# Kernel optimization log

Hardware: AMD Instinct MI355X
Metric: run time of the kernel (lower is better)

Reference implementation:

```python
import jax, jax.numpy as jnp
import numpy as np

N = 50000
E = 800000
IN_CH = 256
HID = 32
HEADS = 4
OUT_CH = 40
NEG_SLOPE = 0.2
BN_EPS = 1e-5


def _gat_conv(x, W, att_src, att_dst, bias, src, dst, num_nodes, concat):
    # x: [N, F_in]; W: [F_in, H*C]; att_src/att_dst: [H, C]
    H, C = att_src.shape
    h = (x @ W).reshape(num_nodes, H, C)            # [N, H, C]
    a_src = (h * att_src[None]).sum(-1)             # [N, H]
    a_dst = (h * att_dst[None]).sum(-1)             # [N, H]
    e = jax.nn.leaky_relu(a_src[src] + a_dst[dst], NEG_SLOPE)  # [Etot, H]
    # segment softmax over incoming edges of each destination node
    m = jax.ops.segment_max(e, dst, num_segments=num_nodes)    # [N, H]
    ex = jnp.exp(e - m[dst])
    s = jax.ops.segment_sum(ex, dst, num_segments=num_nodes)   # [N, H]
    alpha = ex / (s[dst] + 1e-16)                   # [Etot, H]
    out = jax.ops.segment_sum(h[src] * alpha[:, :, None], dst,
                              num_segments=num_nodes)          # [N, H, C]
    out = out.reshape(num_nodes, H * C) if concat else out.mean(axis=1)
    return out + bias


def setup_inputs() -> dict:
    key = jax.random.key(0)
    ks = jax.random.split(key, 12)
    x = jax.random.normal(ks[0], (N, IN_CH), dtype=jnp.float32)
    edge_index = jax.random.randint(ks[1], (2, E), 0, N, dtype=jnp.int64)
    # layer 1: in -> heads*hid, concat
    W1 = jax.random.normal(ks[2], (IN_CH, HEADS * HID), dtype=jnp.float32) * (1.0 / np.sqrt(IN_CH))
    att_src1 = jax.random.normal(ks[3], (HEADS, HID), dtype=jnp.float32) * 0.1
    att_dst1 = jax.random.normal(ks[4], (HEADS, HID), dtype=jnp.float32) * 0.1
    b1 = jnp.zeros((HEADS * HID,), dtype=jnp.float32)
    # batch norm over hidden*heads features
    gamma = jnp.ones((HEADS * HID,), dtype=jnp.float32)
    beta = jnp.zeros((HEADS * HID,), dtype=jnp.float32)
    # layer 2: heads*hid -> out, heads=1, mean (concat=False)
    W2 = jax.random.normal(ks[5], (HEADS * HID, OUT_CH), dtype=jnp.float32) * (1.0 / np.sqrt(HEADS * HID))
    att_src2 = jax.random.normal(ks[6], (1, OUT_CH), dtype=jnp.float32) * 0.1
    att_dst2 = jax.random.normal(ks[7], (1, OUT_CH), dtype=jnp.float32) * 0.1
    b2 = jnp.zeros((OUT_CH,), dtype=jnp.float32)
    return {"x": x, "edge_index": edge_index, "W1": W1, "att_src1": att_src1,
            "att_dst1": att_dst1, "b1": b1, "gamma": gamma, "beta": beta,
            "W2": W2, "att_src2": att_src2, "att_dst2": att_dst2, "b2": b2}


def reference(x, edge_index, W1, att_src1, att_dst1, b1, gamma, beta,
              W2, att_src2, att_dst2, b2):
    num_nodes = x.shape[0]
    loops = jnp.arange(num_nodes, dtype=edge_index.dtype)
    src = jnp.concatenate([edge_index[0], loops])   # add self-loops (PyG default)
    dst = jnp.concatenate([edge_index[1], loops])
    h = _gat_conv(x, W1, att_src1, att_dst1, b1, src, dst, num_nodes, concat=True)
    # BatchNorm over nodes (training-mode batch statistics)
    mu = h.mean(axis=0)
    var = h.var(axis=0)
    h = (h - mu) * jax.lax.rsqrt(var + BN_EPS) * gamma + beta
    h = jax.nn.elu(h)
    out = _gat_conv(h, W2, att_src2, att_dst2, b2, src, dst, num_nodes, concat=False)
    return out
```

## Files before the change

kernel.cpp:

```cpp
#include <hip/hip_runtime.h>

#define NN 50000
#define EE 800000
#define FIN 256
#define F1 128
#define F2 40
#define CAP 48
#define G1B ((NN + 63) / 64)
#define FILLB ((EE + 255) / 256)
#define G1PB 3126
#define G2B ((NN + 15) / 16)
#define LSTR 56

typedef unsigned int u32;
typedef unsigned short u16;
typedef _Float16 h8 __attribute__((ext_vector_type(8)));
typedef float f4 __attribute__((ext_vector_type(4)));

static __device__ __forceinline__ u32 f2bf(float f) {
  u32 u = __float_as_uint(f);
  return (u + 0x7FFFu + ((u >> 16) & 1u)) >> 16;
}
#define BF_LO(u) __uint_as_float((u) << 16)
#define BF_HI(u) __uint_as_float((u) & 0xFFFF0000u)

__global__ __launch_bounds__(256) void g1f_kernel(const float* __restrict__ x,
                                                  const float* __restrict__ W1,
                                                  const float* __restrict__ att_src,
                                                  const float* __restrict__ att_dst,
                                                  u32* __restrict__ h1bf,
                                                  float* __restrict__ a_src,
                                                  float* __restrict__ a_dst,
                                                  const int* __restrict__ ei,
                                                  int* __restrict__ cnt,
                                                  int* __restrict__ csr) {
  __shared__ __align__(16) _Float16 Alds[64 * LSTR];
  __shared__ __align__(16) _Float16 Blds[128 * LSTR];
  const int t = threadIdx.x;

  if (blockIdx.x >= G1B) {
    int e = (blockIdx.x - G1B) * 256 + t;
    if (e < EE) {
      int src = ei[e];
      int dst = ei[EE + e];
      int p = atomicAdd(cnt + dst, 1);
      if (p < CAP) csr[dst * CAP + p] = src;
    }
    return;
  }

  const int m0 = blockIdx.x * 64;
  const int l  = t & 63;
  const int w  = t >> 6;
  const int q  = l & 15;
  const int hq = l >> 4;

  const int arow  = t >> 2;
  const int akoff = (t & 3) * 8;
  const int bn    = t & 127;
  const int bkh   = (t >> 7) * 16;

  f4 acc[8] = {};

  float ax[8];
  float bx[16];
  {
    int gr = m0 + arow;
    if (gr < NN) {
      float4 u0 = *(const float4*)(x + (size_t)gr * FIN + akoff);
      float4 u1 = *(const float4*)(x + (size_t)gr * FIN + akoff + 4);
      ax[0] = u0.x; ax[1] = u0.y; ax[2] = u0.z; ax[3] = u0.w;
      ax[4] = u1.x; ax[5] = u1.y; ax[6] = u1.z; ax[7] = u1.w;
    } else {
#pragma unroll
      for (int i = 0; i < 8; ++i) ax[i] = 0.f;
    }
#pragma unroll
    for (int i = 0; i < 16; ++i) bx[i] = W1[(size_t)(bkh + i) * F1 + bn];
  }

  for (int s = 0; s < 8; ++s) {
    __syncthreads();
    {
      h8 av;
#pragma unroll
      for (int i = 0; i < 8; ++i) av[i] = (_Float16)ax[i];
      *(h8*)(Alds + arow * LSTR + akoff) = av;
      h8 bv0, bv1;
#pragma unroll
      for (int i = 0; i < 8; ++i) { bv0[i] = (_Float16)bx[i]; bv1[i] = (_Float16)bx[8 + i]; }
      *(h8*)(Blds + bn * LSTR + bkh) = bv0;
      *(h8*)(Blds + bn * LSTR + bkh + 8) = bv1;
    }
    __syncthreads();
    if (s < 7) {
      int k0 = (s + 1) * 32;
      int gr = m0 + arow;
      if (gr < NN) {
        float4 u0 = *(const float4*)(x + (size_t)gr * FIN + k0 + akoff);
        float4 u1 = *(const float4*)(x + (size_t)gr * FIN + k0 + akoff + 4);
        ax[0] = u0.x; ax[1] = u0.y; ax[2] = u0.z; ax[3] = u0.w;
        ax[4] = u1.x; ax[5] = u1.y; ax[6] = u1.z; ax[7] = u1.w;
      } else {
#pragma unroll
        for (int i = 0; i < 8; ++i) ax[i] = 0.f;
      }
#pragma unroll
      for (int i = 0; i < 16; ++i) bx[i] = W1[(size_t)(k0 + bkh + i) * F1 + bn];
    }
    h8 af = *(const h8*)(Alds + (w * 16 + q) * LSTR + hq * 8);
#pragma unroll
    for (int nf = 0; nf < 8; ++nf) {
      h8 bf = *(const h8*)(Blds + (nf * 16 + q) * LSTR + hq * 8);
      acc[nf] = __builtin_amdgcn_mfma_f32_16x16x32_f16(af, bf, acc[nf], 0, 0, 0);
    }
  }

  u16* h1u = (u16*)h1bf;
#pragma unroll
  for (int nf = 0; nf < 8; ++nf) {
    int ph = nf >> 1;
#pragma unroll
    for (int r = 0; r < 4; ++r) {
      int grow = m0 + w * 16 + hq * 4 + r;
      if (grow < NN)
        h1u[((size_t)ph * NN + grow) * 32 + (nf & 1) * 16 + q] = (u16)f2bf(acc[nf][r]);
    }
  }
  float as8[8], ad8[8];
#pragma unroll
  for (int nf = 0; nf < 8; ++nf) {
    as8[nf] = att_src[nf * 16 + q];
    ad8[nf] = att_dst[nf * 16 + q];
  }
#pragma unroll
  for (int r = 0; r < 4; ++r) {
    float p0 = acc[0][r] * as8[0] + acc[1][r] * as8[1];
    float p1 = acc[2][r] * as8[2] + acc[3][r] * as8[3];
    float p2 = acc[4][r] * as8[4] + acc[5][r] * as8[5];
    float p3 = acc[6][r] * as8[6] + acc[7][r] * as8[7];
    float d0 = acc[0][r] * ad8[0] + acc[1][r] * ad8[1];
    float d1 = acc[2][r] * ad8[2] + acc[3][r] * ad8[3];
    float d2 = acc[4][r] * ad8[4] + acc[5][r] * ad8[5];
    float d3 = acc[6][r] * ad8[6] + acc[7][r] * ad8[7];
#pragma unroll
    for (int off = 1; off < 16; off <<= 1) {
      p0 += __shfl_xor(p0, off); p1 += __shfl_xor(p1, off);
      p2 += __shfl_xor(p2, off); p3 += __shfl_xor(p3, off);
      d0 += __shfl_xor(d0, off); d1 += __shfl_xor(d1, off);
      d2 += __shfl_xor(d2, off); d3 += __shfl_xor(d3, off);
    }
    int grow = m0 + w * 16 + hq * 4 + r;
    if (grow < NN && q < 8) {
      float vs = (q & 2) ? ((q & 1) ? p3 : p2) : ((q & 1) ? p1 : p0);
      float vd = (q & 2) ? ((q & 1) ? d3 : d2) : ((q & 1) ? d1 : d0);
      if (q < 4) a_src[grow * 4 + q] = vs;
      else       a_dst[grow * 4 + (q - 4)] = vd;
    }
  }
}

__global__ __launch_bounds__(256) void gather1_kernel(const int* __restrict__ cnt,
                                                      const int* __restrict__ csr,
                                                      const float* __restrict__ a_src,
                                                      const float* __restrict__ a_dst,
                                                      const u32* __restrict__ h1bf,
                                                      const float* __restrict__ b1,
                                                      float* __restrict__ h1b,
                                                      float* __restrict__ bnsum,
                                                      float* __restrict__ bnsq) {
  __shared__ float bns[32], bnq[32];
  int t = threadIdx.x;
  if (t < 32) { bns[t] = 0.f; bnq[t] = 0.f; }
  __syncthreads();
  int d = blockIdx.x;
  int xcd = d & 7;
  int p = xcd >> 1;
  int nb = ((d >> 3) << 1) + (xcd & 1);
  int n = nb * 16 + (t >> 4);
  int sub = t & 15;
  int g = sub >> 2;
  int l = sub & 3;
  int f0 = p * 32 + l * 8;
  float acc[8] = {0.f, 0.f, 0.f, 0.f, 0.f, 0.f, 0.f, 0.f};
  float ssum = 0.f;
  if (n < NN) {
    float adst = a_dst[n * 4 + p];
    const u32* hb = h1bf + (size_t)p * NN * 16 + l * 4;
    if (g == 0) {
      float e0 = a_src[n * 4 + p] + adst;
      e0 = e0 > 0.f ? e0 : 0.2f * e0;
      float x0 = __expf(e0);
      uint4 qv = *(const uint4*)(hb + (size_t)n * 16);
      acc[0] = fmaf(x0, BF_LO(qv.x), acc[0]); acc[1] = fmaf(x0, BF_HI(qv.x), acc[1]);
      acc[2] = fmaf(x0, BF_LO(qv.y), acc[2]); acc[3] = fmaf(x0, BF_HI(qv.y), acc[3]);
      acc[4] = fmaf(x0, BF_LO(qv.z), acc[4]); acc[5] = fmaf(x0, BF_HI(qv.z), acc[5]);
      acc[6] = fmaf(x0, BF_LO(qv.w), acc[6]); acc[7] = fmaf(x0, BF_HI(qv.w), acc[7]);
      ssum += x0;
    }
    const int* row = csr + n * CAP;
    int m = cnt[n]; if (m > CAP) m = CAP;
    int i = g;
    for (; i + 4 < m; i += 8) {
      int s0 = row[i];
      int s1 = row[i + 4];
      float e0 = a_src[s0 * 4 + p] + adst;
      float e1 = a_src[s1 * 4 + p] + adst;
      uint4 q0 = *(const uint4*)(hb + (size_t)s0 * 16);
      uint4 q1 = *(const uint4*)(hb + (size_t)s1 * 16);
      e0 = e0 > 0.f ? e0 : 0.2f * e0;  float x0 = __expf(e0);
      e1 = e1 > 0.f ? e1 : 0.2f * e1;  float x1 = __expf(e1);
      acc[0] = fmaf(x0, BF_LO(q0.x), acc[0]); acc[1] = fmaf(x0, BF_HI(q0.x), acc[1]);
      acc[2] = fmaf(x0, BF_LO(q0.y), acc[2]); acc[3] = fmaf(x0, BF_HI(q0.y), acc[3]);
      acc[4] = fmaf(x0, BF_LO(q0.z), acc[4]); acc[5] = fmaf(x0, BF_HI(q0.z), acc[5]);
      acc[6] = fmaf(x0, BF_LO(q0.w), acc[6]); acc[7] = fmaf(x0, BF_HI(q0.w), acc[7]);
      acc[0] = fmaf(x1, BF_LO(q1.x), acc[0]); acc[1] = fmaf(x1, BF_HI(q1.x), acc[1]);
      acc[2] = fmaf(x1, BF_LO(q1.y), acc[2]); acc[3] = fmaf(x1, BF_HI(q1.y), acc[3]);
      acc[4] = fmaf(x1, BF_LO(q1.z), acc[4]); acc[5] = fmaf(x1, BF_HI(q1.z), acc[5]);
      acc[6] = fmaf(x1, BF_LO(q1.w), acc[6]); acc[7] = fmaf(x1, BF_HI(q1.w), acc[7]);
      ssum += x0 + x1;
    }
    for (; i < m; i += 4) {
      int s0 = row[i];
      float e0 = a_src[s0 * 4 + p] + adst;
      e0 = e0 > 0.f ? e0 : 0.2f * e0;
      float x0 = __expf(e0);
      uint4 qv = *(const uint4*)(hb + (size_t)s0 * 16);
      acc[0] = fmaf(x0, BF_LO(qv.x), acc[0]); acc[1] = fmaf(x0, BF_HI(qv.x), acc[1]);
      acc[2] = fmaf(x0, BF_LO(qv.y), acc[2]); acc[3] = fmaf(x0, BF_HI(qv.y), acc[3]);
      acc[4] = fmaf(x0, BF_LO(qv.z), acc[4]); acc[5] = fmaf(x0, BF_HI(qv.z), acc[5]);
      acc[6] = fmaf(x0, BF_LO(qv.w), acc[6]); acc[7] = fmaf(x0, BF_HI(qv.w), acc[7]);
      ssum += x0;
    }
  }
#pragma unroll
  for (int j = 0; j < 8; ++j) {
    acc[j] += __shfl_xor(acc[j], 4);
    acc[j] += __shfl_xor(acc[j], 8);
  }
  ssum += __shfl_xor(ssum, 4);
  ssum += __shfl_xor(ssum, 8);
  if (n < NN && g == 0) {
    float inv = 1.f / (ssum + 1e-16f);
    float4 b0 = *(const float4*)(b1 + f0);
    float4 b4 = *(const float4*)(b1 + f0 + 4);
    float o[8];
    o[0] = acc[0] * inv + b0.x; o[1] = acc[1] * inv + b0.y;
    o[2] = acc[2] * inv + b0.z; o[3] = acc[3] * inv + b0.w;
    o[4] = acc[4] * inv + b4.x; o[5] = acc[5] * inv + b4.y;
    o[6] = acc[6] * inv + b4.z; o[7] = acc[7] * inv + b4.w;
    float4 w0 = {o[0], o[1], o[2], o[3]};
    float4 w1 = {o[4], o[5], o[6], o[7]};
    *(float4*)(h1b + (size_t)n * F1 + f0) = w0;
    *(float4*)(h1b + (size_t)n * F1 + f0 + 4) = w1;
    int lb = l * 8;
#pragma unroll
    for (int j = 0; j < 8; ++j) {
      atomicAdd(&bns[lb + j], o[j]);
      atomicAdd(&bnq[lb + j], o[j] * o[j]);
    }
  }
  __syncthreads();
  if (t < 32) {
    atomicAdd(bnsum + p * 32 + t, bns[t]);
    atomicAdd(bnsq + p * 32 + t, bnq[t]);
  }
}

__global__ __launch_bounds__(256) void gemm2_kernel(const float* __restrict__ hpre,
                                                    const float* __restrict__ W2,
                                                    const float* __restrict__ bnsum,
                                                    const float* __restrict__ bnsq,
                                                    const float* __restrict__ gamma,
                                                    const float* __restrict__ beta,
                                                    u16* __restrict__ h2a,
                                                    u16* __restrict__ h2b,
                                                    const float* __restrict__ att_src2,
                                                    const float* __restrict__ att_dst2,
                                                    float* __restrict__ a_src2,
                                                    float* __restrict__ a_dst2) {
  __shared__ float Wlds[128 * 40];
  __shared__ float Alds[16 * 128];
  __shared__ float sc[128], sh[128];
  int t = threadIdx.x;
  for (int i = t; i < 128 * 40; i += 256) Wlds[i] = W2[i];
  if (t < 128) {
    const float invN = 1.f / (float)NN;
    float mu = bnsum[t] * invN;
    float var = bnsq[t] * invN - mu * mu;
    float s = gamma[t] * rsqrtf(var + 1e-5f);
    sc[t] = s;
    sh[t] = beta[t] - mu * s;
  }
  int tr = t >> 3;
  int tc = t & 7;
  float as5[5], ad5[5];
#pragma unroll
  for (int j = 0; j < 5; ++j) { as5[j] = att_src2[tc * 5 + j]; ad5[j] = att_dst2[tc * 5 + j]; }
  int n0 = blockIdx.x * 128;
  int lrow = t >> 1;
  int lkk = (t & 1) * 8;
  float acc[4][5];
#pragma unroll
  for (int i = 0; i < 4; ++i)
#pragma unroll
    for (int j = 0; j < 5; ++j) acc[i][j] = 0.f;

  for (int k0 = 0; k0 < F1; k0 += 16) {
    float av[8];
    int gn = n0 + lrow;
    if (gn < NN) {
      float4 v0 = *(const float4*)(hpre + (size_t)gn * F1 + k0 + lkk);
      float4 v1 = *(const float4*)(hpre + (size_t)gn * F1 + k0 + lkk + 4);
      av[0] = v0.x; av[1] = v0.y; av[2] = v0.z; av[3] = v0.w;
      av[4] = v1.x; av[5] = v1.y; av[6] = v1.z; av[7] = v1.w;
    } else {
#pragma unroll
      for (int j = 0; j < 8; ++j) av[j] = 0.f;
    }
    __syncthreads();
#pragma unroll
    for (int j = 0; j < 8; ++j) {
      int kg = k0 + lkk + j;
      float a = av[j] * sc[kg] + sh[kg];
      a = a > 0.f ? a : (__expf(a) - 1.f);
      Alds[(lkk + j) * 128 + lrow] = a;
    }
    __syncthreads();
#pragma unroll
    for (int k = 0; k < 16; ++k) {
      float4 a4 = *(const float4*)(Alds + k * 128 + tr * 4);
      float aa[4] = {a4.x, a4.y, a4.z, a4.w};
      float w[5];
#pragma unroll
      for (int j = 0; j < 5; ++j) w[j] = Wlds[(k0 + k) * 40 + tc * 5 + j];
#pragma unroll
      for (int i = 0; i < 4; ++i)
#pragma unroll
        for (int j = 0; j < 5; ++j) acc[i][j] = fmaf(aa[i], w[j], acc[i][j]);
    }
  }
#pragma unroll
  for (int i = 0; i < 4; ++i) {
    int gn = n0 + tr * 4 + i;
    if (gn < NN) {
#pragma unroll
      for (int j = 0; j < 5; ++j) {
        int f = tc * 5 + j;
        u16 v = (u16)f2bf(acc[i][j]);
        if (f < 32) h2a[(size_t)gn * 32 + f] = v;
        else        h2b[(size_t)gn * 8 + (f - 32)] = v;
      }
    }
  }
#pragma unroll
  for (int i = 0; i < 4; ++i) {
    float ps = 0.f, pd = 0.f;
#pragma unroll
    for (int j = 0; j < 5; ++j) { ps += acc[i][j] * as5[j]; pd += acc[i][j] * ad5[j]; }
#pragma unroll
    for (int off = 1; off < 8; off <<= 1) {
      ps += __shfl_xor(ps, off);
      pd += __shfl_xor(pd, off);
    }
    if (tc == 0) {
      int gn = n0 + tr * 4 + i;
      if (gn < NN) { a_src2[gn] = ps; a_dst2[gn] = pd; }
    }
  }
}

__global__ __launch_bounds__(256) void gather2_kernel(const int* __restrict__ cnt,
                                                      const int* __restrict__ csr,
                                                      const float* __restrict__ a_src,
                                                      const float* __restrict__ a_dst,
                                                      const u32* __restrict__ h2a,
                                                      const u32* __restrict__ h2b,
                                                      const float* __restrict__ b2,
                                                      float* __restrict__ out) {
  int t = threadIdx.x;
  int n = blockIdx.x * 16 + (t >> 4);
  if (n >= NN) return;
  int l = t & 7;
  int g = (t >> 3) & 1;
  bool act = (l < 5);
  bool isA = (l < 4);
  float adst = a_dst[n];
  float acc[8] = {0.f, 0.f, 0.f, 0.f, 0.f, 0.f, 0.f, 0.f};
  float ssum = 0.f;
  const uint4 zz = {0u, 0u, 0u, 0u};
  if (g == 0) {
    float e0 = a_src[n] + adst;
    e0 = e0 > 0.f ? e0 : 0.2f * e0;
    float x0 = __expf(e0);
    uint4 q = act ? (isA ? *(const uint4*)(h2a + (size_t)n * 16 + l * 4)
                         : *(const uint4*)(h2b + (size_t)n * 4)) : zz;
    acc[0] = fmaf(x0, BF_LO(q.x), acc[0]); acc[1] = fmaf(x0, BF_HI(q.x), acc[1]);
    acc[2] = fmaf(x0, BF_LO(q.y), acc[2]); acc[3] = fmaf(x0, BF_HI(q.y), acc[3]);
    acc[4] = fmaf(x0, BF_LO(q.z), acc[4]); acc[5] = fmaf(x0, BF_HI(q.z), acc[5]);
    acc[6] = fmaf(x0, BF_LO(q.w), acc[6]); acc[7] = fmaf(x0, BF_HI(q.w), acc[7]);
    ssum += x0;
  }
  const int* row = csr + n * CAP;
  int m = cnt[n]; if (m > CAP) m = CAP;
  for (int c = 4 * g; c < m; c += 8) {
    if (c + 4 <= m) {
      int4 s4 = *(const int4*)(row + c);
      float e0 = a_src[s4.x] + adst;
      float e1 = a_src[s4.y] + adst;
      float e2 = a_src[s4.z] + adst;
      float e3 = a_src[s4.w] + adst;
      uint4 q0 = act ? (isA ? *(const uint4*)(h2a + (size_t)s4.x * 16 + l * 4)
                            : *(const uint4*)(h2b + (size_t)s4.x * 4)) : zz;
      uint4 q1 = act ? (isA ? *(const uint4*)(h2a + (size_t)s4.y * 16 + l * 4)
                            : *(const uint4*)(h2b + (size_t)s4.y * 4)) : zz;
      uint4 q2 = act ? (isA ? *(const uint4*)(h2a + (size_t)s4.z * 16 + l * 4)
                            : *(const uint4*)(h2b + (size_t)s4.z * 4)) : zz;
      uint4 q3 = act ? (isA ? *(const uint4*)(h2a + (size_t)s4.w * 16 + l * 4)
                            : *(const uint4*)(h2b + (size_t)s4.w * 4)) : zz;
      e0 = e0 > 0.f ? e0 : 0.2f * e0;  float x0 = __expf(e0);
      e1 = e1 > 0.f ? e1 : 0.2f * e1;  float x1 = __expf(e1);
      e2 = e2 > 0.f ? e2 : 0.2f * e2;  float x2 = __expf(e2);
      e3 = e3 > 0.f ? e3 : 0.2f * e3;  float x3 = __expf(e3);
      acc[0] = fmaf(x0, BF_LO(q0.x), acc[0]); acc[1] = fmaf(x0, BF_HI(q0.x), acc[1]);
      acc[2] = fmaf(x0, BF_LO(q0.y), acc[2]); acc[3] = fmaf(x0, BF_HI(q0.y), acc[3]);
      acc[4] = fmaf(x0, BF_LO(q0.z), acc[4]); acc[5] = fmaf(x0, BF_HI(q0.z), acc[5]);
      acc[6] = fmaf(x0, BF_LO(q0.w), acc[6]); acc[7] = fmaf(x0, BF_HI(q0.w), acc[7]);
      acc[0] = fmaf(x1, BF_LO(q1.x), acc[0]); acc[1] = fmaf(x1, BF_HI(q1.x), acc[1]);
      acc[2] = fmaf(x1, BF_LO(q1.y), acc[2]); acc[3] = fmaf(x1, BF_HI(q1.y), acc[3]);
      acc[4] = fmaf(x1, BF_LO(q1.z), acc[4]); acc[5] = fmaf(x1, BF_HI(q1.z), acc[5]);
      acc[6] = fmaf(x1, BF_LO(q1.w), acc[6]); acc[7] = fmaf(x1, BF_HI(q1.w), acc[7]);
      acc[0] = fmaf(x2, BF_LO(q2.x), acc[0]); acc[1] = fmaf(x2, BF_HI(q2.x), acc[1]);
      acc[2] = fmaf(x2, BF_LO(q2.y), acc[2]); acc[3] = fmaf(x2, BF_HI(q2.y), acc[3]);
      acc[4] = fmaf(x2, BF_LO(q2.z), acc[4]); acc[5] = fmaf(x2, BF_HI(q2.z), acc[5]);
      acc[6] = fmaf(x2, BF_LO(q2.w), acc[6]); acc[7] = fmaf(x2, BF_HI(q2.w), acc[7]);
      acc[0] = fmaf(x3, BF_LO(q3.x), acc[0]); acc[1] = fmaf(x3, BF_HI(q3.x), acc[1]);
      acc[2] = fmaf(x3, BF_LO(q3.y), acc[2]); acc[3] = fmaf(x3, BF_HI(q3.y), acc[3]);
      acc[4] = fmaf(x3, BF_LO(q3.z), acc[4]); acc[5] = fmaf(x3, BF_HI(q3.z), acc[5]);
      acc[6] = fmaf(x3, BF_LO(q3.w), acc[6]); acc[7] = fmaf(x3, BF_HI(q3.w), acc[7]);
      ssum += x0 + x1 + x2 + x3;
    } else {
      for (int i = c; i < m; ++i) {
        int s0 = row[i];
        float e0 = a_src[s0] + adst;
        e0 = e0 > 0.f ? e0 : 0.2f * e0;
        float x0 = __expf(e0);
        uint4 q = act ? (isA ? *(const uint4*)(h2a + (size_t)s0 * 16 + l * 4)
                             : *(const uint4*)(h2b + (size_t)s0 * 4)) : zz;
        acc[0] = fmaf(x0, BF_LO(q.x), acc[0]); acc[1] = fmaf(x0, BF_HI(q.x), acc[1]);
        acc[2] = fmaf(x0, BF_LO(q.y), acc[2]); acc[3] = fmaf(x0, BF_HI(q.y), acc[3]);
        acc[4] = fmaf(x0, BF_LO(q.z), acc[4]); acc[5] = fmaf(x0, BF_HI(q.z), acc[5]);
        acc[6] = fmaf(x0, BF_LO(q.w), acc[6]); acc[7] = fmaf(x0, BF_HI(q.w), acc[7]);
        ssum += x0;
      }
    }
  }
#pragma unroll
  for (int j = 0; j < 8; ++j) acc[j] += __shfl_xor(acc[j], 8);
  ssum += __shfl_xor(ssum, 8);
  float inv = 1.f / (ssum + 1e-16f);
  if (g == 0 && act) {
    float* op = out + (size_t)n * F2 + l * 8;
#pragma unroll
    for (int j = 0; j < 8; ++j) op[j] = acc[j] * inv + b2[l * 8 + j];
  }
}

extern "C" void kernel_launch(void* const* d_in, const int* in_sizes, int n_in,
                              void* d_out, int out_size, void* d_ws, size_t ws_size,
                              hipStream_t stream) {
  const float* x        = (const float*)d_in[0];
  const int*   ei       = (const int*)d_in[1];
  const float* W1       = (const float*)d_in[2];
  const float* att_src1 = (const float*)d_in[3];
  const float* att_dst1 = (const float*)d_in[4];
  const float* b1       = (const float*)d_in[5];
  const float* gamma    = (const float*)d_in[6];
  const float* beta     = (const float*)d_in[7];
  const float* W2       = (const float*)d_in[8];
  const float* att_src2 = (const float*)d_in[9];
  const float* att_dst2 = (const float*)d_in[10];
  const float* b2       = (const float*)d_in[11];
  float* out = (float*)d_out;

  int* cnt      = (int*)d_ws;
  float* bnsum  = (float*)(cnt + 50048);
  float* bnsq   = bnsum + 128;
  int* csr      = (int*)(bnsq + 128);
  u32* h1bf     = (u32*)(csr + NN * CAP);
  float* h1b    = (float*)(h1bf + 3200000);
  u32* h2a      = (u32*)(h1b + 6400000);
  u32* h2b      = h2a + 800000;
  float* a_src1 = (float*)(h2b + 200000);
  float* a_dst1 = a_src1 + 200000;
  float* a_src2 = a_dst1 + 200000;
  float* a_dst2 = a_src2 + 50000;

  hipMemsetAsync(cnt, 0, (50048 + 256) * sizeof(int), stream);

  g1f_kernel<<<G1B + FILLB, 256, 0, stream>>>(x, W1, att_src1, att_dst1,
                                              h1bf, a_src1, a_dst1,
                                              ei, cnt, csr);
  gather1_kernel<<<(G1PB / 2) * 8, 256, 0, stream>>>(cnt, csr, a_src1, a_dst1,
                                                     h1bf, b1, h1b, bnsum, bnsq);
  gemm2_kernel<<<(NN + 127) / 128, 256, 0, stream>>>(h1b, W2, bnsum, bnsq,
                                                     gamma, beta,
                                                     (u16*)h2a, (u16*)h2b,
                                                     att_src2, att_dst2,
                                                     a_src2, a_dst2);
  gather2_kernel<<<G2B, 256, 0, stream>>>(cnt, csr, a_src2, a_dst2,
                                          h2a, h2b, b2, out);
}
```

Before: 313.1 us.

## Store layer-1 features row-major and gather all heads per node in one block

```diff
diff --git a/kernel.cpp b/kernel.cpp
--- a/kernel.cpp
+++ b/kernel.cpp
@@ -8,7 +8,6 @@
 #define CAP 48
 #define G1B ((NN + 63) / 64)
 #define FILLB ((EE + 255) / 256)
-#define G1PB 3126
 #define G2B ((NN + 15) / 16)
 #define LSTR 56
 
@@ -23,6 +22,12 @@
 }
 #define BF_LO(u) __uint_as_float((u) << 16)
 #define BF_HI(u) __uint_as_float((u) & 0xFFFF0000u)
+
+static __device__ __forceinline__ float sel4(float4 v, int h) {
+  float a = (h & 1) ? v.y : v.x;
+  float b = (h & 1) ? v.w : v.z;
+  return (h & 2) ? b : a;
+}
 
 __global__ __launch_bounds__(256) void g1f_kernel(const float* __restrict__ x,
                                                   const float* __restrict__ W1,
@@ -119,12 +124,11 @@
   u16* h1u = (u16*)h1bf;
 #pragma unroll
   for (int nf = 0; nf < 8; ++nf) {
-    int ph = nf >> 1;
 #pragma unroll
     for (int r = 0; r < 4; ++r) {
       int grow = m0 + w * 16 + hq * 4 + r;
       if (grow < NN)
-        h1u[((size_t)ph * NN + grow) * 32 + (nf & 1) * 16 + q] = (u16)f2bf(acc[nf][r]);
+        h1u[(size_t)grow * 128 + nf * 16 + q] = (u16)f2bf(acc[nf][r]);
     }
   }
   float as8[8], ad8[8];
@@ -169,101 +173,86 @@
                                                       float* __restrict__ h1b,
                                                       float* __restrict__ bnsum,
                                                       float* __restrict__ bnsq) {
-  __shared__ float bns[32], bnq[32];
+  __shared__ float bns[128], bnq[128];
   int t = threadIdx.x;
-  if (t < 32) { bns[t] = 0.f; bnq[t] = 0.f; }
+  if (t < 128) { bns[t] = 0.f; bnq[t] = 0.f; }
   __syncthreads();
-  int d = blockIdx.x;
-  int xcd = d & 7;
-  int p = xcd >> 1;
-  int nb = ((d >> 3) << 1) + (xcd & 1);
-  int n = nb * 16 + (t >> 4);
-  int sub = t & 15;
-  int g = sub >> 2;
-  int l = sub & 3;
-  int f0 = p * 32 + l * 8;
+  int n = blockIdx.x * 16 + (t >> 4);
+  int l = t & 15;
+  int h = l >> 2;
+  float adst = sel4(*(const float4*)(a_dst + n * 4), h);
   float acc[8] = {0.f, 0.f, 0.f, 0.f, 0.f, 0.f, 0.f, 0.f};
   float ssum = 0.f;
-  if (n < NN) {
-    float adst = a_dst[n * 4 + p];
-    const u32* hb = h1bf + (size_t)p * NN * 16 + l * 4;
-    if (g == 0) {
-      float e0 = a_src[n * 4 + p] + adst;
-      e0 = e0 > 0.f ? e0 : 0.2f * e0;
-      float x0 = __expf(e0);
-      uint4 qv = *(const uint4*)(hb + (size_t)n * 16);
-      acc[0] = fmaf(x0, BF_LO(qv.x), acc[0]); acc[1] = fmaf(x0, BF_HI(qv.x), acc[1]);
-      acc[2] = fmaf(x0, BF_LO(qv.y), acc[2]); acc[3] = fmaf(x0, BF_HI(qv.y), acc[3]);
-      acc[4] = fmaf(x0, BF_LO(qv.z), acc[4]); acc[5] = fmaf(x0, BF_HI(qv.z), acc[5]);
-      acc[6] = fmaf(x0, BF_LO(qv.w), acc[6]); acc[7] = fmaf(x0, BF_HI(qv.w), acc[7]);
-      ssum += x0;
-    }
-    const int* row = csr + n * CAP;
-    int m = cnt[n]; if (m > CAP) m = CAP;
-    int i = g;
-    for (; i + 4 < m; i += 8) {
-      int s0 = row[i];
-      int s1 = row[i + 4];
-      float e0 = a_src[s0 * 4 + p] + adst;
-      float e1 = a_src[s1 * 4 + p] + adst;
-      uint4 q0 = *(const uint4*)(hb + (size_t)s0 * 16);
-      uint4 q1 = *(const uint4*)(hb + (size_t)s1 * 16);
-      e0 = e0 > 0.f ? e0 : 0.2f * e0;  float x0 = __expf(e0);
-      e1 = e1 > 0.f ? e1 : 0.2f * e1;  float x1 = __expf(e1);
-      acc[0] = fmaf(x0, BF_LO(q0.x), acc[0]); acc[1] = fmaf(x0, BF_HI(q0.x), acc[1]);
-      acc[2] = fmaf(x0, BF_LO(q0.y), acc[2]); acc[3] = fmaf(x0, BF_HI(q0.y), acc[3]);
-      acc[4] = fmaf(x0, BF_LO(q0.z), acc[4]); acc[5] = fmaf(x0, BF_HI(q0.z), acc[5]);
-      acc[6] = fmaf(x0, BF_LO(q0.w), acc[6]); acc[7] = fmaf(x0, BF_HI(q0.w), acc[7]);
-      acc[0] = fmaf(x1, BF_LO(q1.x), acc[0]); acc[1] = fmaf(x1, BF_HI(q1.x), acc[1]);
-      acc[2] = fmaf(x1, BF_LO(q1.y), acc[2]); acc[3] = fmaf(x1, BF_HI(q1.y), acc[3]);
-      acc[4] = fmaf(x1, BF_LO(q1.z), acc[4]); acc[5] = fmaf(x1, BF_HI(q1.z), acc[5]);
-      acc[6] = fmaf(x1, BF_LO(q1.w), acc[6]); acc[7] = fmaf(x1, BF_HI(q1.w), acc[7]);
-      ssum += x0 + x1;
-    }
-    for (; i < m; i += 4) {
-      int s0 = row[i];
-      float e0 = a_src[s0 * 4 + p] + adst;
-      e0 = e0 > 0.f ? e0 : 0.2f * e0;
-      float x0 = __expf(e0);
-      uint4 qv = *(const uint4*)(hb + (size_t)s0 * 16);
-      acc[0] = fmaf(x0, BF_LO(qv.x), acc[0]); acc[1] = fmaf(x0, BF_HI(qv.x), acc[1]);
-      acc[2] = fmaf(x0, BF_LO(qv.y), acc[2]); acc[3] = fmaf(x0, BF_HI(qv.y), acc[3]);
-      acc[4] = fmaf(x0, BF_LO(qv.z), acc[4]); acc[5] = fmaf(x0, BF_HI(qv.z), acc[5]);
-      acc[6] = fmaf(x0, BF_LO(qv.w), acc[6]); acc[7] = fmaf(x0, BF_HI(qv.w), acc[7]);
-      ssum += x0;
-    }
-  }
+  const u32* hb = h1bf + l * 4;
+  {
+    float e0 = sel4(*(const float4*)(a_src + n * 4), h) + adst;
+    e0 = e0 > 0.f ? e0 : 0.2f * e0;
+    float x0 = __expf(e0);
+    uint4 qv = *(const uint4*)(hb + (size_t)n * 64);
+    acc[0] = fmaf(x0, BF_LO(qv.x), acc[0]); acc[1] = fmaf(x0, BF_HI(qv.x), acc[1]);
+    acc[2] = fmaf(x0, BF_LO(qv.y), acc[2]); acc[3] = fmaf(x0, BF_HI(qv.y), acc[3]);
+    acc[4] = fmaf(x0, BF_LO(qv.z), acc[4]); acc[5] = fmaf(x0, BF_HI(qv.z), acc[5]);
+    acc[6] = fmaf(x0, BF_LO(qv.w), acc[6]); acc[7] = fmaf(x0, BF_HI(qv.w), acc[7]);
+    ssum += x0;
+  }
+  const int* row = csr + n * CAP;
+  int m = cnt[n]; if (m > CAP) m = CAP;
+  int i = 0;
+  for (; i + 1 < m; i += 2) {
+    int s0 = row[i];
+    int s1 = row[i + 1];
+    float4 v0 = *(const float4*)(a_src + s0 * 4);
+    float4 v1 = *(const float4*)(a_src + s1 * 4);
+    uint4 q0 = *(const uint4*)(hb + (size_t)s0 * 64);
+    uint4 q1 = *(const uint4*)(hb + (size_t)s1 * 64);
+    float e0 = sel4(v0, h) + adst;
+    float e1 = sel4(v1, h) + adst;
+    e0 = e0 > 0.f ? e0 : 0.2f * e0;  float x0 = __expf(e0);
+    e1 = e1 > 0.f ? e1 : 0.2f * e1;  float x1 = __expf(e1);
+    acc[0] = fmaf(x0, BF_LO(q0.x), acc[0]); acc[1] = fmaf(x0, BF_HI(q0.x), acc[1]);
+    acc[2] = fmaf(x0, BF_LO(q0.y), acc[2]); acc[3] = fmaf(x0, BF_HI(q0.y), acc[3]);
+    acc[4] = fmaf(x0, BF_LO(q0.z), acc[4]); acc[5] = fmaf(x0, BF_HI(q0.z), acc[5]);
+    acc[6] = fmaf(x0, BF_LO(q0.w), acc[6]); acc[7] = fmaf(x0, BF_HI(q0.w), acc[7]);
+    acc[0] = fmaf(x1, BF_LO(q1.x), acc[0]); acc[1] = fmaf(x1, BF_HI(q1.x), acc[1]);
+    acc[2] = fmaf(x1, BF_LO(q1.y), acc[2]); acc[3] = fmaf(x1, BF_HI(q1.y), acc[3]);
+    acc[4] = fmaf(x1, BF_LO(q1.z), acc[4]); acc[5] = fmaf(x1, BF_HI(q1.z), acc[5]);
+    acc[6] = fmaf(x1, BF_LO(q1.w), acc[6]); acc[7] = fmaf(x1, BF_HI(q1.w), acc[7]);
+    ssum += x0 + x1;
+  }
+  if (i < m) {
+    int s0 = row[i];
+    float e0 = sel4(*(const float4*)(a_src + s0 * 4), h) + adst;
+    e0 = e0 > 0.f ? e0 : 0.2f * e0;
+    float x0 = __expf(e0);
+    uint4 qv = *(const uint4*)(hb + (size_t)s0 * 64);
+    acc[0] = fmaf(x0, BF_LO(qv.x), acc[0]); acc[1] = fmaf(x0, BF_HI(qv.x), acc[1]);
+    acc[2] = fmaf(x0, BF_LO(qv.y), acc[2]); acc[3] = fmaf(x0, BF_HI(qv.y), acc[3]);
+    acc[4] = fmaf(x0, BF_LO(qv.z), acc[4]); acc[5] = fmaf(x0, BF_HI(qv.z), acc[5]);
+    acc[6] = fmaf(x0, BF_LO(qv.w), acc[6]); acc[7] = fmaf(x0, BF_HI(qv.w), acc[7]);
+    ssum += x0;
+  }
+  float inv = 1.f / (ssum + 1e-16f);
+  int f0 = l * 8;
+  float4 b0 = *(const float4*)(b1 + f0);
+  float4 b4 = *(const float4*)(b1 + f0 + 4);
+  float o[8];
+  o[0] = acc[0] * inv + b0.x; o[1] = acc[1] * inv + b0.y;
+  o[2] = acc[2] * inv + b0.z; o[3] = acc[3] * inv + b0.w;
+  o[4] = acc[4] * inv + b4.x; o[5] = acc[5] * inv + b4.y;
+  o[6] = acc[6] * inv + b4.z; o[7] = acc[7] * inv + b4.w;
+  float4 w0 = {o[0], o[1], o[2], o[3]};
+  float4 w1 = {o[4], o[5], o[6], o[7]};
+  *(float4*)(h1b + (size_t)n * F1 + f0) = w0;
+  *(float4*)(h1b + (size_t)n * F1 + f0 + 4) = w1;
 #pragma unroll
   for (int j = 0; j < 8; ++j) {
-    acc[j] += __shfl_xor(acc[j], 4);
-    acc[j] += __shfl_xor(acc[j], 8);
-  }
-  ssum += __shfl_xor(ssum, 4);
-  ssum += __shfl_xor(ssum, 8);
-  if (n < NN && g == 0) {
-    float inv = 1.f / (ssum + 1e-16f);
-    float4 b0 = *(const float4*)(b1 + f0);
-    float4 b4 = *(const float4*)(b1 + f0 + 4);
-    float o[8];
-    o[0] = acc[0] * inv + b0.x; o[1] = acc[1] * inv + b0.y;
-    o[2] = acc[2] * inv + b0.z; o[3] = acc[3] * inv + b0.w;
-    o[4] = acc[4] * inv + b4.x; o[5] = acc[5] * inv + b4.y;
-    o[6] = acc[6] * inv + b4.z; o[7] = acc[7] * inv + b4.w;
-    float4 w0 = {o[0], o[1], o[2], o[3]};
-    float4 w1 = {o[4], o[5], o[6], o[7]};
-    *(float4*)(h1b + (size_t)n * F1 + f0) = w0;
-    *(float4*)(h1b + (size_t)n * F1 + f0 + 4) = w1;
-    int lb = l * 8;
-#pragma unroll
-    for (int j = 0; j < 8; ++j) {
-      atomicAdd(&bns[lb + j], o[j]);
-      atomicAdd(&bnq[lb + j], o[j] * o[j]);
-    }
+    atomicAdd(&bns[f0 + j], o[j]);
+    atomicAdd(&bnq[f0 + j], o[j] * o[j]);
   }
   __syncthreads();
-  if (t < 32) {
-    atomicAdd(bnsum + p * 32 + t, bns[t]);
-    atomicAdd(bnsq + p * 32 + t, bnq[t]);
+  if (t < 128) {
+    atomicAdd(bnsum + t, bns[t]);
+    atomicAdd(bnsq + t, bnq[t]);
   }
 }
 
@@ -501,8 +490,8 @@
   g1f_kernel<<<G1B + FILLB, 256, 0, stream>>>(x, W1, att_src1, att_dst1,
                                               h1bf, a_src1, a_dst1,
                                               ei, cnt, csr);
-  gather1_kernel<<<(G1PB / 2) * 8, 256, 0, stream>>>(cnt, csr, a_src1, a_dst1,
-                                                     h1bf, b1, h1b, bnsum, bnsq);
+  gather1_kernel<<<G2B, 256, 0, stream>>>(cnt, csr, a_src1, a_dst1,
+                                          h1bf, b1, h1b, bnsum, bnsq);
   gemm2_kernel<<<(NN + 127) / 128, 256, 0, stream>>>(h1b, W2, bnsum, bnsq,
                                                      gamma, beta,
                                                      (u16*)h2a, (u16*)h2b,
```

Result: slower. 332.4 us (+6.2%).

## Compress CSR indices to 16-bit and split gather2 into head and tail block types

Applied to the files above, without the earlier changes.

```diff
diff --git a/kernel.cpp b/kernel.cpp
--- a/kernel.cpp
+++ b/kernel.cpp
@@ -9,7 +9,8 @@
 #define G1B ((NN + 63) / 64)
 #define FILLB ((EE + 255) / 256)
 #define G1PB 3126
-#define G2B ((NN + 15) / 16)
+#define G2P0 3125
+#define G2P1 ((NN + 63) / 64)
 #define LSTR 56
 
 typedef unsigned int u32;
@@ -33,7 +34,7 @@
                                                   float* __restrict__ a_dst,
                                                   const int* __restrict__ ei,
                                                   int* __restrict__ cnt,
-                                                  int* __restrict__ csr) {
+                                                  u16* __restrict__ csr) {
   __shared__ __align__(16) _Float16 Alds[64 * LSTR];
   __shared__ __align__(16) _Float16 Blds[128 * LSTR];
   const int t = threadIdx.x;
@@ -44,7 +45,7 @@
       int src = ei[e];
       int dst = ei[EE + e];
       int p = atomicAdd(cnt + dst, 1);
-      if (p < CAP) csr[dst * CAP + p] = src;
+      if (p < CAP) csr[dst * CAP + p] = (u16)src;
     }
     return;
   }
@@ -161,7 +162,7 @@
 }
 
 __global__ __launch_bounds__(256) void gather1_kernel(const int* __restrict__ cnt,
-                                                      const int* __restrict__ csr,
+                                                      const u16* __restrict__ csr,
                                                       const float* __restrict__ a_src,
                                                       const float* __restrict__ a_dst,
                                                       const u32* __restrict__ h1bf,
@@ -198,18 +199,18 @@
       acc[6] = fmaf(x0, BF_LO(qv.w), acc[6]); acc[7] = fmaf(x0, BF_HI(qv.w), acc[7]);
       ssum += x0;
     }
-    const int* row = csr + n * CAP;
+    const u16* row = csr + (size_t)n * CAP;
     int m = cnt[n]; if (m > CAP) m = CAP;
     int i = g;
     for (; i + 4 < m; i += 8) {
       int s0 = row[i];
       int s1 = row[i + 4];
-      float e0 = a_src[s0 * 4 + p] + adst;
-      float e1 = a_src[s1 * 4 + p] + adst;
+      float e0 = a_src[s0 * 4 + p];
+      float e1 = a_src[s1 * 4 + p];
       uint4 q0 = *(const uint4*)(hb + (size_t)s0 * 16);
       uint4 q1 = *(const uint4*)(hb + (size_t)s1 * 16);
-      e0 = e0 > 0.f ? e0 : 0.2f * e0;  float x0 = __expf(e0);
-      e1 = e1 > 0.f ? e1 : 0.2f * e1;  float x1 = __expf(e1);
+      e0 += adst; e0 = e0 > 0.f ? e0 : 0.2f * e0;  float x0 = __expf(e0);
+      e1 += adst; e1 = e1 > 0.f ? e1 : 0.2f * e1;  float x1 = __expf(e1);
       acc[0] = fmaf(x0, BF_LO(q0.x), acc[0]); acc[1] = fmaf(x0, BF_HI(q0.x), acc[1]);
       acc[2] = fmaf(x0, BF_LO(q0.y), acc[2]); acc[3] = fmaf(x0, BF_HI(q0.y), acc[3]);
       acc[4] = fmaf(x0, BF_LO(q0.z), acc[4]); acc[5] = fmaf(x0, BF_HI(q0.z), acc[5]);
@@ -371,7 +372,7 @@
 }
 
 __global__ __launch_bounds__(256) void gather2_kernel(const int* __restrict__ cnt,
-                                                      const int* __restrict__ csr,
+                                                      const u16* __restrict__ csr,
                                                       const float* __restrict__ a_src,
                                                       const float* __restrict__ a_dst,
                                                       const u32* __restrict__ h2a,
@@ -379,49 +380,39 @@
                                                       const float* __restrict__ b2,
                                                       float* __restrict__ out) {
   int t = threadIdx.x;
-  int n = blockIdx.x * 16 + (t >> 4);
-  if (n >= NN) return;
-  int l = t & 7;
-  int g = (t >> 3) & 1;
-  bool act = (l < 5);
-  bool isA = (l < 4);
-  float adst = a_dst[n];
-  float acc[8] = {0.f, 0.f, 0.f, 0.f, 0.f, 0.f, 0.f, 0.f};
-  float ssum = 0.f;
-  const uint4 zz = {0u, 0u, 0u, 0u};
-  if (g == 0) {
-    float e0 = a_src[n] + adst;
-    e0 = e0 > 0.f ? e0 : 0.2f * e0;
-    float x0 = __expf(e0);
-    uint4 q = act ? (isA ? *(const uint4*)(h2a + (size_t)n * 16 + l * 4)
-                         : *(const uint4*)(h2b + (size_t)n * 4)) : zz;
-    acc[0] = fmaf(x0, BF_LO(q.x), acc[0]); acc[1] = fmaf(x0, BF_HI(q.x), acc[1]);
-    acc[2] = fmaf(x0, BF_LO(q.y), acc[2]); acc[3] = fmaf(x0, BF_HI(q.y), acc[3]);
-    acc[4] = fmaf(x0, BF_LO(q.z), acc[4]); acc[5] = fmaf(x0, BF_HI(q.z), acc[5]);
-    acc[6] = fmaf(x0, BF_LO(q.w), acc[6]); acc[7] = fmaf(x0, BF_HI(q.w), acc[7]);
-    ssum += x0;
-  }
-  const int* row = csr + n * CAP;
-  int m = cnt[n]; if (m > CAP) m = CAP;
-  for (int c = 4 * g; c < m; c += 8) {
-    if (c + 4 <= m) {
-      int4 s4 = *(const int4*)(row + c);
-      float e0 = a_src[s4.x] + adst;
-      float e1 = a_src[s4.y] + adst;
-      float e2 = a_src[s4.z] + adst;
-      float e3 = a_src[s4.w] + adst;
-      uint4 q0 = act ? (isA ? *(const uint4*)(h2a + (size_t)s4.x * 16 + l * 4)
-                            : *(const uint4*)(h2b + (size_t)s4.x * 4)) : zz;
-      uint4 q1 = act ? (isA ? *(const uint4*)(h2a + (size_t)s4.y * 16 + l * 4)
-                            : *(const uint4*)(h2b + (size_t)s4.y * 4)) : zz;
-      uint4 q2 = act ? (isA ? *(const uint4*)(h2a + (size_t)s4.z * 16 + l * 4)
-                            : *(const uint4*)(h2b + (size_t)s4.z * 4)) : zz;
-      uint4 q3 = act ? (isA ? *(const uint4*)(h2a + (size_t)s4.w * 16 + l * 4)
-                            : *(const uint4*)(h2b + (size_t)s4.w * 4)) : zz;
-      e0 = e0 > 0.f ? e0 : 0.2f * e0;  float x0 = __expf(e0);
-      e1 = e1 > 0.f ? e1 : 0.2f * e1;  float x1 = __expf(e1);
-      e2 = e2 > 0.f ? e2 : 0.2f * e2;  float x2 = __expf(e2);
-      e3 = e3 > 0.f ? e3 : 0.2f * e3;  float x3 = __expf(e3);
+  int d = blockIdx.x;
+  if (d < G2P0) {
+    int n = d * 16 + (t >> 4);
+    int sub = t & 15;
+    int g = sub >> 2;
+    int l = sub & 3;
+    float adst = a_dst[n];
+    const u32* hb = h2a + l * 4;
+    float acc[8] = {0.f, 0.f, 0.f, 0.f, 0.f, 0.f, 0.f, 0.f};
+    float ssum = 0.f;
+    if (g == 0) {
+      float e0 = a_src[n] + adst;
+      e0 = e0 > 0.f ? e0 : 0.2f * e0;
+      float x0 = __expf(e0);
+      uint4 qv = *(const uint4*)(hb + (size_t)n * 16);
+      acc[0] = fmaf(x0, BF_LO(qv.x), acc[0]); acc[1] = fmaf(x0, BF_HI(qv.x), acc[1]);
+      acc[2] = fmaf(x0, BF_LO(qv.y), acc[2]); acc[3] = fmaf(x0, BF_HI(qv.y), acc[3]);
+      acc[4] = fmaf(x0, BF_LO(qv.z), acc[4]); acc[5] = fmaf(x0, BF_HI(qv.z), acc[5]);
+      acc[6] = fmaf(x0, BF_LO(qv.w), acc[6]); acc[7] = fmaf(x0, BF_HI(qv.w), acc[7]);
+      ssum += x0;
+    }
+    const u16* row = csr + (size_t)n * CAP;
+    int m = cnt[n]; if (m > CAP) m = CAP;
+    int i = g;
+    for (; i + 4 < m; i += 8) {
+      int s0 = row[i];
+      int s1 = row[i + 4];
+      float e0 = a_src[s0];
+      float e1 = a_src[s1];
+      uint4 q0 = *(const uint4*)(hb + (size_t)s0 * 16);
+      uint4 q1 = *(const uint4*)(hb + (size_t)s1 * 16);
+      e0 += adst; e0 = e0 > 0.f ? e0 : 0.2f * e0;  float x0 = __expf(e0);
+      e1 += adst; e1 = e1 > 0.f ? e1 : 0.2f * e1;  float x1 = __expf(e1);
       acc[0] = fmaf(x0, BF_LO(q0.x), acc[0]); acc[1] = fmaf(x0, BF_HI(q0.x), acc[1]);
       acc[2] = fmaf(x0, BF_LO(q0.y), acc[2]); acc[3] = fmaf(x0, BF_HI(q0.y), acc[3]);
       acc[4] = fmaf(x0, BF_LO(q0.z), acc[4]); acc[5] = fmaf(x0, BF_HI(q0.z), acc[5]);
@@ -430,39 +421,110 @@
       acc[2] = fmaf(x1, BF_LO(q1.y), acc[2]); acc[3] = fmaf(x1, BF_HI(q1.y), acc[3]);
       acc[4] = fmaf(x1, BF_LO(q1.z), acc[4]); acc[5] = fmaf(x1, BF_HI(q1.z), acc[5]);
       acc[6] = fmaf(x1, BF_LO(q1.w), acc[6]); acc[7] = fmaf(x1, BF_HI(q1.w), acc[7]);
-      acc[0] = fmaf(x2, BF_LO(q2.x), acc[0]); acc[1] = fmaf(x2, BF_HI(q2.x), acc[1]);
-      acc[2] = fmaf(x2, BF_LO(q2.y), acc[2]); acc[3] = fmaf(x2, BF_HI(q2.y), acc[3]);
-      acc[4] = fmaf(x2, BF_LO(q2.z), acc[4]); acc[5] = fmaf(x2, BF_HI(q2.z), acc[5]);
-      acc[6] = fmaf(x2, BF_LO(q2.w), acc[6]); acc[7] = fmaf(x2, BF_HI(q2.w), acc[7]);
-      acc[0] = fmaf(x3, BF_LO(q3.x), acc[0]); acc[1] = fmaf(x3, BF_HI(q3.x), acc[1]);
-      acc[2] = fmaf(x3, BF_LO(q3.y), acc[2]); acc[3] = fmaf(x3, BF_HI(q3.y), acc[3]);
-      acc[4] = fmaf(x3, BF_LO(q3.z), acc[4]); acc[5] = fmaf(x3, BF_HI(q3.z), acc[5]);
-      acc[6] = fmaf(x3, BF_LO(q3.w), acc[6]); acc[7] = fmaf(x3, BF_HI(q3.w), acc[7]);
-      ssum += x0 + x1 + x2 + x3;
-    } else {
-      for (int i = c; i < m; ++i) {
+      ssum += x0 + x1;
+    }
+    for (; i < m; i += 4) {
+      int s0 = row[i];
+      float e0 = a_src[s0] + adst;
+      e0 = e0 > 0.f ? e0 : 0.2f * e0;
+      float x0 = __expf(e0);
+      uint4 qv = *(const uint4*)(hb + (size_t)s0 * 16);
+      acc[0] = fmaf(x0, BF_LO(qv.x), acc[0]); acc[1] = fmaf(x0, BF_HI(qv.x), acc[1]);
+      acc[2] = fmaf(x0, BF_LO(qv.y), acc[2]); acc[3] = fmaf(x0, BF_HI(qv.y), acc[3]);
+      acc[4] = fmaf(x0, BF_LO(qv.z), acc[4]); acc[5] = fmaf(x0, BF_HI(qv.z), acc[5]);
+      acc[6] = fmaf(x0, BF_LO(qv.w), acc[6]); acc[7] = fmaf(x0, BF_HI(qv.w), acc[7]);
+      ssum += x0;
+    }
+#pragma unroll
+    for (int j = 0; j < 8; ++j) {
+      acc[j] += __shfl_xor(acc[j], 4);
+      acc[j] += __shfl_xor(acc[j], 8);
+    }
+    ssum += __shfl_xor(ssum, 4);
+    ssum += __shfl_xor(ssum, 8);
+    if (g == 0) {
+      float inv = 1.f / (ssum + 1e-16f);
+      int f0 = l * 8;
+      float4 b0 = *(const float4*)(b2 + f0);
+      float4 b4 = *(const float4*)(b2 + f0 + 4);
+      float4 w0 = {acc[0] * inv + b0.x, acc[1] * inv + b0.y,
+                   acc[2] * inv + b0.z, acc[3] * inv + b0.w};
+      float4 w1 = {acc[4] * inv + b4.x, acc[5] * inv + b4.y,
+                   acc[6] * inv + b4.z, acc[7] * inv + b4.w};
+      *(float4*)(out + (size_t)n * F2 + f0) = w0;
+      *(float4*)(out + (size_t)n * F2 + f0 + 4) = w1;
+    }
+  } else {
+    int n = (d - G2P0) * 64 + (t >> 2);
+    int g = t & 3;
+    float acc[8] = {0.f, 0.f, 0.f, 0.f, 0.f, 0.f, 0.f, 0.f};
+    float ssum = 0.f;
+    if (n < NN) {
+      float adst = a_dst[n];
+      if (g == 0) {
+        float e0 = a_src[n] + adst;
+        e0 = e0 > 0.f ? e0 : 0.2f * e0;
+        float x0 = __expf(e0);
+        uint4 qv = *(const uint4*)(h2b + (size_t)n * 4);
+        acc[0] = fmaf(x0, BF_LO(qv.x), acc[0]); acc[1] = fmaf(x0, BF_HI(qv.x), acc[1]);
+        acc[2] = fmaf(x0, BF_LO(qv.y), acc[2]); acc[3] = fmaf(x0, BF_HI(qv.y), acc[3]);
+        acc[4] = fmaf(x0, BF_LO(qv.z), acc[4]); acc[5] = fmaf(x0, BF_HI(qv.z), acc[5]);
+        acc[6] = fmaf(x0, BF_LO(qv.w), acc[6]); acc[7] = fmaf(x0, BF_HI(qv.w), acc[7]);
+        ssum += x0;
+      }
+      const u16* row = csr + (size_t)n * CAP;
+      int m = cnt[n]; if (m > CAP) m = CAP;
+      int i = g;
+      for (; i + 4 < m; i += 8) {
+        int s0 = row[i];
+        int s1 = row[i + 4];
+        float e0 = a_src[s0];
+        float e1 = a_src[s1];
+        uint4 q0 = *(const uint4*)(h2b + (size_t)s0 * 4);
+        uint4 q1 = *(const uint4*)(h2b + (size_t)s1 * 4);
+        e0 += adst; e0 = e0 > 0.f ? e0 : 0.2f * e0;  float x0 = __expf(e0);
+        e1 += adst; e1 = e1 > 0.f ? e1 : 0.2f * e1;  float x1 = __expf(e1);
+        acc[0] = fmaf(x0, BF_LO(q0.x), acc[0]); acc[1] = fmaf(x0, BF_HI(q0.x), acc[1]);
+        acc[2] = fmaf(x0, BF_LO(q0.y), acc[2]); acc[3] = fmaf(x0, BF_HI(q0.y), acc[3]);
+        acc[4] = fmaf(x0, BF_LO(q0.z), acc[4]); acc[5] = fmaf(x0, BF_HI(q0.z), acc[5]);
+        acc[6] = fmaf(x0, BF_LO(q0.w), acc[6]); acc[7] = fmaf(x0, BF_HI(q0.w), acc[7]);
+        acc[0] = fmaf(x1, BF_LO(q1.x), acc[0]); acc[1] = fmaf(x1, BF_HI(q1.x), acc[1]);
+        acc[2] = fmaf(x1, BF_LO(q1.y), acc[2]); acc[3] = fmaf(x1, BF_HI(q1.y), acc[3]);
+        acc[4] = fmaf(x1, BF_LO(q1.z), acc[4]); acc[5] = fmaf(x1, BF_HI(q1.z), acc[5]);
+        acc[6] = fmaf(x1, BF_LO(q1.w), acc[6]); acc[7] = fmaf(x1, BF_HI(q1.w), acc[7]);
+        ssum += x0 + x1;
+      }
+      for (; i < m; i += 4) {
         int s0 = row[i];
         float e0 = a_src[s0] + adst;
         e0 = e0 > 0.f ? e0 : 0.2f * e0;
         float x0 = __expf(e0);
-        uint4 q = act ? (isA ? *(const uint4*)(h2a + (size_t)s0 * 16 + l * 4)
-                             : *(const uint4*)(h2b + (size_t)s0 * 4)) : zz;
-        acc[0] = fmaf(x0, BF_LO(q.x), acc[0]); acc[1] = fmaf(x0, BF_HI(q.x), acc[1]);
-        acc[2] = fmaf(x0, BF_LO(q.y), acc[2]); acc[3] = fmaf(x0, BF_HI(q.y), acc[3]);
-        acc[4] = fmaf(x0, BF_LO(q.z), acc[4]); acc[5] = fmaf(x0, BF_HI(q.z), acc[5]);
-        acc[6] = fmaf(x0, BF_LO(q.w), acc[6]); acc[7] = fmaf(x0, BF_HI(q.w), acc[7]);
+        uint4 qv = *(const uint4*)(h2b + (size_t)s0 * 4);
+        acc[0] = fmaf(x0, BF_LO(qv.x), acc[0]); acc[1] = fmaf(x0, BF_HI(qv.x), acc[1]);
+        acc[2] = fmaf(x0, BF_LO(qv.y), acc[2]); acc[3] = fmaf(x0, BF_HI(qv.y), acc[3]);
+        acc[4] = fmaf(x0, BF_LO(qv.z), acc[4]); acc[5] = fmaf(x0, BF_HI(qv.z), acc[5]);
+        acc[6] = fmaf(x0, BF_LO(qv.w), acc[6]); acc[7] = fmaf(x0, BF_HI(qv.w), acc[7]);
         ssum += x0;
       }
     }
-  }
-#pragma unroll
-  for (int j = 0; j < 8; ++j) acc[j] += __shfl_xor(acc[j], 8);
-  ssum += __shfl_xor(ssum, 8);
-  float inv = 1.f / (ssum + 1e-16f);
-  if (g == 0 && act) {
-    float* op = out + (size_t)n * F2 + l * 8;
-#pragma unroll
-    for (int j = 0; j < 8; ++j) op[j] = acc[j] * inv + b2[l * 8 + j];
+#pragma unroll
+    for (int j = 0; j < 8; ++j) {
+      acc[j] += __shfl_xor(acc[j], 1);
+      acc[j] += __shfl_xor(acc[j], 2);
+    }
+    ssum += __shfl_xor(ssum, 1);
+    ssum += __shfl_xor(ssum, 2);
+    if (n < NN && g == 0) {
+      float inv = 1.f / (ssum + 1e-16f);
+      float4 b0 = *(const float4*)(b2 + 32);
+      float4 b4 = *(const float4*)(b2 + 36);
+      float4 w0 = {acc[0] * inv + b0.x, acc[1] * inv + b0.y,
+                   acc[2] * inv + b0.z, acc[3] * inv + b0.w};
+      float4 w1 = {acc[4] * inv + b4.x, acc[5] * inv + b4.y,
+                   acc[6] * inv + b4.z, acc[7] * inv + b4.w};
+      *(float4*)(out + (size_t)n * F2 + 32) = w0;
+      *(float4*)(out + (size_t)n * F2 + 36) = w1;
+    }
   }
 }
 
@@ -486,8 +548,8 @@
   int* cnt      = (int*)d_ws;
   float* bnsum  = (float*)(cnt + 50048);
   float* bnsq   = bnsum + 128;
-  int* csr      = (int*)(bnsq + 128);
-  u32* h1bf     = (u32*)(csr + NN * CAP);
+  u16* csr      = (u16*)(bnsq + 128);
+  u32* h1bf     = (u32*)(csr + (size_t)NN * CAP);
   float* h1b    = (float*)(h1bf + 3200000);
   u32* h2a      = (u32*)(h1b + 6400000);
   u32* h2b      = h2a + 800000;
@@ -508,6 +570,6 @@
                                                      (u16*)h2a, (u16*)h2b,
                                                      att_src2, att_dst2,
                                                      a_src2, a_dst2);
-  gather2_kernel<<<G2B, 256, 0, stream>>>(cnt, csr, a_src2, a_dst2,
-                                          h2a, h2b, b2, out);
+  gather2_kernel<<<G2P0 + G2P1, 256, 0, stream>>>(cnt, csr, a_src2, a_dst2,
+                                                  h2a, h2b, b2, out);
 }
```

New measurement: 290.2 us. -7.3%, faster.
